# Kernel tuning notes

Measured on AMD Instinct MI355X. Metric: run time of the kernel, lower is better.

## Reference

```python
import jax, jax.numpy as jnp
import numpy as np

B, S, H, T = 64, 512, 768, 9


def setup_inputs() -> dict:
    key = jax.random.key(0)
    ks = jax.random.split(key, 8)
    embeddings = jax.random.normal(ks[0], (B, S, H), dtype=jnp.float32)
    # variable-length mask (first token always valid), as token_type_ids would give
    lengths = jax.random.randint(ks[1], (B,), 1, S + 1)
    mask = (jnp.arange(S)[None, :] < lengths[:, None]).astype(jnp.int32)
    labels = jax.random.randint(ks[2], (B, S), 0, T)
    W = jax.random.normal(ks[3], (T, H), dtype=jnp.float32) * (1.0 / np.sqrt(H))
    b = jnp.zeros((T,), dtype=jnp.float32)
    start_trans = jax.random.normal(ks[4], (T,), dtype=jnp.float32) * 0.1
    transitions = jax.random.normal(ks[5], (T, T), dtype=jnp.float32) * 0.1
    end_trans = jax.random.normal(ks[6], (T,), dtype=jnp.float32) * 0.1
    return {"embeddings": embeddings, "W": W, "b": b,
            "start_trans": start_trans, "transitions": transitions,
            "end_trans": end_trans, "labels": labels, "mask": mask}


def _crf_nll(emissions, labels, mask_bool, start_trans, transitions, end_trans):
    # emissions: [B,S,T]; returns negative log-likelihood per sequence [B]
    Bn = emissions.shape[0]
    mask_f = mask_bool.astype(emissions.dtype)
    # --- gold path score (numerator) ---
    first = start_trans[labels[:, 0]] + emissions[jnp.arange(Bn), 0, labels[:, 0]]
    emis_sc = jnp.take_along_axis(emissions, labels[..., None], axis=2)[..., 0]  # [B,S]
    trans_sc = transitions[labels[:, :-1], labels[:, 1:]]                         # [B,S-1]
    num = first + jnp.sum((emis_sc[:, 1:] + trans_sc) * mask_f[:, 1:], axis=1)
    last_idx = jnp.sum(mask_bool.astype(jnp.int32), axis=1) - 1
    last_lab = jnp.take_along_axis(labels, last_idx[:, None], axis=1)[:, 0]
    num = num + end_trans[last_lab]
    # --- log partition (forward algorithm, logsumexp recurrence) ---
    alpha0 = start_trans[None, :] + emissions[:, 0]          # [B,T]
    em_t = jnp.swapaxes(emissions, 0, 1)[1:]                 # [S-1,B,T]
    m_t = mask_bool.T[1:]                                    # [S-1,B]
    def step(alpha, xs):
        em, m = xs
        new = jax.nn.logsumexp(alpha[:, :, None] + transitions[None], axis=1) + em
        return jnp.where(m[:, None], new, alpha), None
    alpha, _ = jax.lax.scan(step, alpha0, (em_t, m_t))
    denom = jax.nn.logsumexp(alpha + end_trans[None, :], axis=1)
    return denom - num


def reference(embeddings, W, b, start_trans, transitions, end_trans, labels, mask):
    # dropout is identity at eval; Linear + ReLU emissions
    emissions = jax.nn.relu(jnp.einsum('bsh,th->bst', embeddings, W) + b)
    # -100 padding handling: zero out mask there, clamp labels to 0
    valid = labels != -100
    mask_bool = (mask != 0) & valid
    labels_mod = jnp.where(valid, labels, 0)
    nll = _crf_nll(emissions, labels_mod, mask_bool, start_trans, transitions, end_trans)
    return jnp.mean(nll)  # == -loss.mean() of the log-likelihood
```

## Files before the change

### kernel.cpp

```cpp
#include <hip/hip_runtime.h>

#define NEG_INF (-1e30f)

static constexpr int Bn = 64;
static constexpr int Sn = 512;
static constexpr int Hn = 768;
static constexpr int Tn = 9;
static constexpr int KC = 32;
static constexpr int CL = 16;
static constexpr int PSTRIDE = 108;

__device__ __forceinline__ float dot4(float4 a, float4 b) {
    return a.x * b.x + a.y * b.y + a.z * b.z + a.w * b.w;
}

__global__ __launch_bounds__(128) void fused_chunk_kernel(
        const float* __restrict__ emb, const float* __restrict__ Wm,
        const float* __restrict__ bias, const float* __restrict__ trans,
        const int* __restrict__ labels, const int* __restrict__ mask,
        float* __restrict__ chunkP, float* __restrict__ auxN,
        int* __restrict__ auxC) {
    const int bk = blockIdx.x;
    const int b  = bk >> 5;
    const int k  = bk & 31;
    const int t0 = 1 + k * CL;
    const int tid  = threadIdx.x;
    const int w    = tid >> 6;
    const int lane = tid & 63;

    __shared__ float em_s[CL][Tn];
    __shared__ int   on_s[CL];
    __shared__ float tr_s[81];

    float4 wr[Tn][3];
#pragma unroll
    for (int t = 0; t < Tn; ++t) {
        const float4* w4 = (const float4*)(Wm + t * Hn);
#pragma unroll
        for (int i = 0; i < 3; ++i) wr[t][i] = w4[lane + (i << 6)];
    }
    float bb[Tn];
#pragma unroll
    for (int t = 0; t < Tn; ++t) bb[t] = bias[t];

    if (tid < 81) tr_s[tid] = trans[tid];

    int myLab = 0, myLabP = 0, myOn = 0;
    if (tid < CL) {
        int t = t0 + tid;
        if (t < Sn) {
            int lb = labels[b * Sn + t];
            int lp = labels[b * Sn + t - 1];
            int mm = mask[b * Sn + t];
            myOn  = (mm != 0) && (lb != -100);
            myLab = (lb == -100) ? 0 : lb;
            myLabP = (lp == -100) ? 0 : lp;
        }
        on_s[tid] = myOn;
    }

#pragma unroll
    for (int rr = 0; rr < 8; ++rr) {
        const int r = w * 8 + rr;
        const int t = t0 + r;
        const int trow = (t < Sn) ? t : (Sn - 1);
        const float4* e4 = (const float4*)(emb + ((size_t)b * Sn + trow) * Hn);
        float4 e0 = e4[lane];
        float4 e1 = e4[lane + 64];
        float4 e2 = e4[lane + 128];
        float acc[Tn];
#pragma unroll
        for (int t9 = 0; t9 < Tn; ++t9)
            acc[t9] = dot4(e0, wr[t9][0]) + dot4(e1, wr[t9][1]) + dot4(e2, wr[t9][2]);
#pragma unroll
        for (int t9 = 0; t9 < Tn; ++t9) {
#pragma unroll
            for (int off = 32; off; off >>= 1)
                acc[t9] += __shfl_xor(acc[t9], off);
        }
        if (lane == 0) {
#pragma unroll
            for (int t9 = 0; t9 < Tn; ++t9)
                em_s[r][t9] = fmaxf(acc[t9] + bb[t9], 0.0f);
        }
    }
    __syncthreads();

    float nump = 0.0f;
    int cnt = 0;
    if (tid < CL && myOn) {
        nump = em_s[tid][myLab] + tr_s[myLabP * Tn + myLab];
        cnt = 1;
    }
    if (w == 0) {
#pragma unroll
        for (int off = 8; off; off >>= 1) {
            nump += __shfl_xor(nump, off);
            cnt  += __shfl_xor(cnt, off);
        }
        if (lane == 0) { auxN[bk] = nump; auxC[bk] = cnt; }
    }

    const int v  = lane / 9;
    const int jj = lane - v * 9;
    const bool act = lane < ((w == 0) ? 45 : 36);
    const int rid = (w == 0) ? v : (5 + v);

    float c[Tn];
#pragma unroll
    for (int kk = 0; kk < Tn; ++kk) c[kk] = tr_s[kk * Tn + jj];

    float pv = (act && rid == jj) ? 0.0f : NEG_INF;

    for (int u = 0; u < CL; ++u) {
        if (!on_s[u]) continue;
        float x[Tn];
#pragma unroll
        for (int kk = 0; kk < Tn; ++kk) {
            float a = __shfl(pv, (v * Tn + kk) & 63);
            x[kk] = a + c[kk];
        }
        float mx = x[0];
#pragma unroll
        for (int kk = 1; kk < Tn; ++kk) mx = fmaxf(mx, x[kk]);
        float s = 0.0f;
#pragma unroll
        for (int kk = 0; kk < Tn; ++kk) s += __expf(x[kk] - mx);
        float nv = mx + __logf(s) + em_s[u][jj];
        pv = act ? nv : pv;
    }
    if (act) chunkP[(size_t)bk * PSTRIDE + jj * 12 + rid] = pv;
}

__global__ __launch_bounds__(64) void combine_kernel(
        const float* __restrict__ emb, const float* __restrict__ Wm,
        const float* __restrict__ bias, const float* __restrict__ startT,
        const float* __restrict__ endT, const int* __restrict__ labels,
        const int* __restrict__ mask, const float* __restrict__ chunkP,
        const float* __restrict__ auxN, const int* __restrict__ auxC,
        float* __restrict__ nll) {
    const int b = blockIdx.x;
    const int lane = threadIdx.x;

    float4 wr[Tn][3];
#pragma unroll
    for (int t = 0; t < Tn; ++t) {
        const float4* w4 = (const float4*)(Wm + t * Hn);
#pragma unroll
        for (int i = 0; i < 3; ++i) wr[t][i] = w4[lane + (i << 6)];
    }
    const float4* e4 = (const float4*)(emb + (size_t)b * Sn * Hn);
    float4 e0 = e4[lane];
    float4 e1 = e4[lane + 64];
    float4 e2 = e4[lane + 128];
    float acc[Tn];
#pragma unroll
    for (int t = 0; t < Tn; ++t)
        acc[t] = dot4(e0, wr[t][0]) + dot4(e1, wr[t][1]) + dot4(e2, wr[t][2]);
#pragma unroll
    for (int t = 0; t < Tn; ++t) {
#pragma unroll
        for (int off = 32; off; off >>= 1)
            acc[t] += __shfl_xor(acc[t], off);
    }
    float em0 = NEG_INF;
#pragma unroll
    for (int t = 0; t < Tn; ++t) {
        float vt = fmaxf(acc[t] + bias[t], 0.0f);
        if (lane == t) em0 = vt;
    }
    float alpha = (lane < Tn) ? (startT[lane] + em0) : NEG_INF;

    int lab0r = labels[b * Sn];
    int lab0 = (lab0r == -100) ? 0 : lab0r;
    float first = startT[lab0] + __shfl(em0, lab0);

    float numP = (lane < KC) ? auxN[b * KC + lane] : 0.0f;
    int   cntP = (lane < KC) ? auxC[b * KC + lane] : 0;
#pragma unroll
    for (int off = 32; off; off >>= 1) {
        numP += __shfl_xor(numP, off);
        cntP += __shfl_xor(cntP, off);
    }
    int m0 = ((mask[b * Sn] != 0) && (lab0r != -100)) ? 1 : 0;
    int cntTot = cntP + m0;
    int lastIdx = cntTot - 1;
    if (lastIdx < 0) lastIdx = 0;
    int lastLab = labels[b * Sn + lastIdx];
    lastLab = (lastLab == -100) ? 0 : lastLab;
    float num = first + numP + endT[lastLab];

    const float* Pb = chunkP + (size_t)b * KC * PSTRIDE;
    float4 p0 = make_float4(0, 0, 0, 0), p1 = p0, p2 = p0;
    if (lane < Tn) {
        const float4* pp = (const float4*)(Pb + lane * 12);
        p0 = pp[0]; p1 = pp[1]; p2 = pp[2];
    }
    for (int k = 0; k < KC; ++k) {
        float4 q0 = p0, q1 = p1, q2 = p2;
        if (k + 1 < KC && lane < Tn) {
            const float4* pp = (const float4*)(Pb + (size_t)(k + 1) * PSTRIDE + lane * 12);
            p0 = pp[0]; p1 = pp[1]; p2 = pp[2];
        }
        float av[Tn];
#pragma unroll
        for (int i = 0; i < Tn; ++i) av[i] = __shfl(alpha, i);
        float x[Tn];
        x[0] = av[0] + q0.x; x[1] = av[1] + q0.y; x[2] = av[2] + q0.z;
        x[3] = av[3] + q0.w; x[4] = av[4] + q1.x; x[5] = av[5] + q1.y;
        x[6] = av[6] + q1.z; x[7] = av[7] + q1.w; x[8] = av[8] + q2.x;
        float mx = x[0];
#pragma unroll
        for (int i = 1; i < Tn; ++i) mx = fmaxf(mx, x[i]);
        float s = 0.0f;
#pragma unroll
        for (int i = 0; i < Tn; ++i) s += __expf(x[i] - mx);
        float na = mx + __logf(s);
        alpha = (lane < Tn) ? na : NEG_INF;
    }

    float z = (lane < Tn) ? (alpha + endT[lane]) : NEG_INF;
    float mx = z;
#pragma unroll
    for (int off = 32; off; off >>= 1) mx = fmaxf(mx, __shfl_xor(mx, off));
    float s = __expf(z - mx);
#pragma unroll
    for (int off = 32; off; off >>= 1) s += __shfl_xor(s, off);
    float denom = mx + __logf(s);

    if (lane == 0) nll[b] = denom - num;
}

__global__ __launch_bounds__(64) void mean_kernel(const float* __restrict__ nll,
        float* __restrict__ out) {
    float v = nll[threadIdx.x];
#pragma unroll
    for (int off = 32; off; off >>= 1) v += __shfl_xor(v, off);
    if (threadIdx.x == 0) out[0] = v * (1.0f / 64.0f);
}

extern "C" void kernel_launch(void* const* d_in, const int* in_sizes, int n_in,
                              void* d_out, int out_size, void* d_ws, size_t ws_size,
                              hipStream_t stream) {
    const float* emb    = (const float*)d_in[0];
    const float* Wm     = (const float*)d_in[1];
    const float* bias   = (const float*)d_in[2];
    const float* startT = (const float*)d_in[3];
    const float* trans  = (const float*)d_in[4];
    const float* endT   = (const float*)d_in[5];
    const int*   labels = (const int*)d_in[6];
    const int*   mask   = (const int*)d_in[7];

    float* chunkP = (float*)d_ws;
    float* auxN   = chunkP + (size_t)Bn * KC * PSTRIDE;
    int*   auxC   = (int*)(auxN + (size_t)Bn * KC);
    float* nll    = (float*)(auxC + (size_t)Bn * KC);
    float* out    = (float*)d_out;

    fused_chunk_kernel<<<Bn * KC, 128, 0, stream>>>(emb, Wm, bias, trans,
                                                    labels, mask, chunkP, auxN, auxC);
    combine_kernel<<<Bn, 64, 0, stream>>>(emb, Wm, bias, startT, endT,
                                          labels, mask, chunkP, auxN, auxC, nll);
    mean_kernel<<<1, 64, 0, stream>>>(nll, out);
}
```

Baseline: 61.05 us.

## Split emission GEMV into persistent prefetching kernel separate from CRF chunk scan

Moves the Linear+ReLU emission computation out of the chunked CRF kernel into a dedicated persistent kernel. Each wave loads W into registers once, handles two tokens per iteration, and software-prefetches the next pair's embeddings. The emissions go to a workspace buffer that the chunk and combine kernels read back. This trades an extra launch and a small emission round-trip through memory for better streaming of the 100MB embedding read and less repeated W loading.

```diff
diff --git a/kernel.cpp b/kernel.cpp
--- a/kernel.cpp
+++ b/kernel.cpp
@@ -14,12 +14,75 @@
     return a.x * b.x + a.y * b.y + a.z * b.z + a.w * b.w;
 }
 
-__global__ __launch_bounds__(128) void fused_chunk_kernel(
-        const float* __restrict__ emb, const float* __restrict__ Wm,
-        const float* __restrict__ bias, const float* __restrict__ trans,
-        const int* __restrict__ labels, const int* __restrict__ mask,
-        float* __restrict__ chunkP, float* __restrict__ auxN,
-        int* __restrict__ auxC) {
+__global__ __launch_bounds__(256) void emis_kernel(const float* __restrict__ emb,
+        const float* __restrict__ Wm, const float* __restrict__ bias,
+        float* __restrict__ em) {
+    const int lane = threadIdx.x & 63;
+    const int gw = (blockIdx.x * 256 + threadIdx.x) >> 6;
+    const int nw = (gridDim.x * 256) >> 6;
+    const int NP = (Bn * Sn) >> 1;
+
+    float4 w[Tn][3];
+#pragma unroll
+    for (int t = 0; t < Tn; ++t) {
+        const float4* w4 = (const float4*)(Wm + t * Hn);
+#pragma unroll
+        for (int i = 0; i < 3; ++i) w[t][i] = w4[lane + (i << 6)];
+    }
+    float bb[Tn];
+#pragma unroll
+    for (int t = 0; t < Tn; ++t) bb[t] = bias[t];
+
+    const int sub = (lane < 9) ? lane : (lane - 9);
+
+    float4 cA0, cA1, cA2, cB0, cB1, cB2;
+    int p = gw;
+    if (p < NP) {
+        const float4* a4 = (const float4*)(emb + (size_t)(2 * p) * Hn);
+        cA0 = a4[lane]; cA1 = a4[lane + 64]; cA2 = a4[lane + 128];
+        cB0 = a4[lane + 192]; cB1 = a4[lane + 256]; cB2 = a4[lane + 320];
+    }
+    while (p < NP) {
+        const int pn = p + nw;
+        float4 nA0, nA1, nA2, nB0, nB1, nB2;
+        if (pn < NP) {
+            const float4* a4 = (const float4*)(emb + (size_t)(2 * pn) * Hn);
+            nA0 = a4[lane]; nA1 = a4[lane + 64]; nA2 = a4[lane + 128];
+            nB0 = a4[lane + 192]; nB1 = a4[lane + 256]; nB2 = a4[lane + 320];
+        }
+        float accA[Tn], accB[Tn];
+#pragma unroll
+        for (int t = 0; t < Tn; ++t) {
+            accA[t] = dot4(cA0, w[t][0]) + dot4(cA1, w[t][1]) + dot4(cA2, w[t][2]);
+            accB[t] = dot4(cB0, w[t][0]) + dot4(cB1, w[t][1]) + dot4(cB2, w[t][2]);
+        }
+#pragma unroll
+        for (int off = 32; off; off >>= 1) {
+#pragma unroll
+            for (int t = 0; t < Tn; ++t) {
+                accA[t] += __shfl_xor(accA[t], off);
+                accB[t] += __shfl_xor(accB[t], off);
+            }
+        }
+        float outv = 0.0f;
+#pragma unroll
+        for (int t = 0; t < Tn; ++t) {
+            float va = fmaxf(accA[t] + bb[t], 0.0f);
+            float vb = fmaxf(accB[t] + bb[t], 0.0f);
+            float sel = (lane < 9) ? va : vb;
+            outv = (sub == t) ? sel : outv;
+        }
+        if (lane < 18) em[(size_t)(2 * p) * Tn + lane] = outv;
+        p = pn;
+        cA0 = nA0; cA1 = nA1; cA2 = nA2;
+        cB0 = nB0; cB1 = nB1; cB2 = nB2;
+    }
+}
+
+__global__ __launch_bounds__(128) void chunk_kernel(const float* __restrict__ em,
+        const float* __restrict__ trans, const int* __restrict__ labels,
+        const int* __restrict__ mask, float* __restrict__ chunkP,
+        float* __restrict__ auxN, int* __restrict__ auxC) {
     const int bk = blockIdx.x;
     const int b  = bk >> 5;
     const int k  = bk & 31;
@@ -31,17 +94,6 @@
     __shared__ float em_s[CL][Tn];
     __shared__ int   on_s[CL];
     __shared__ float tr_s[81];
-
-    float4 wr[Tn][3];
-#pragma unroll
-    for (int t = 0; t < Tn; ++t) {
-        const float4* w4 = (const float4*)(Wm + t * Hn);
-#pragma unroll
-        for (int i = 0; i < 3; ++i) wr[t][i] = w4[lane + (i << 6)];
-    }
-    float bb[Tn];
-#pragma unroll
-    for (int t = 0; t < Tn; ++t) bb[t] = bias[t];
 
     if (tid < 81) tr_s[tid] = trans[tid];
 
@@ -58,31 +110,10 @@
         }
         on_s[tid] = myOn;
     }
-
-#pragma unroll
-    for (int rr = 0; rr < 8; ++rr) {
-        const int r = w * 8 + rr;
-        const int t = t0 + r;
-        const int trow = (t < Sn) ? t : (Sn - 1);
-        const float4* e4 = (const float4*)(emb + ((size_t)b * Sn + trow) * Hn);
-        float4 e0 = e4[lane];
-        float4 e1 = e4[lane + 64];
-        float4 e2 = e4[lane + 128];
-        float acc[Tn];
-#pragma unroll
-        for (int t9 = 0; t9 < Tn; ++t9)
-            acc[t9] = dot4(e0, wr[t9][0]) + dot4(e1, wr[t9][1]) + dot4(e2, wr[t9][2]);
-#pragma unroll
-        for (int t9 = 0; t9 < Tn; ++t9) {
-#pragma unroll
-            for (int off = 32; off; off >>= 1)
-                acc[t9] += __shfl_xor(acc[t9], off);
-        }
-        if (lane == 0) {
-#pragma unroll
-            for (int t9 = 0; t9 < Tn; ++t9)
-                em_s[r][t9] = fmaxf(acc[t9] + bb[t9], 0.0f);
-        }
+    {
+        const int nst = (Sn - t0 < CL) ? (Sn - t0) : CL;
+        const float* src = em + (size_t)(b * Sn + t0) * Tn;
+        for (int u = tid; u < nst * Tn; u += 128) ((float*)em_s)[u] = src[u];
     }
     __syncthreads();
 
@@ -132,43 +163,15 @@
     if (act) chunkP[(size_t)bk * PSTRIDE + jj * 12 + rid] = pv;
 }
 
-__global__ __launch_bounds__(64) void combine_kernel(
-        const float* __restrict__ emb, const float* __restrict__ Wm,
-        const float* __restrict__ bias, const float* __restrict__ startT,
-        const float* __restrict__ endT, const int* __restrict__ labels,
-        const int* __restrict__ mask, const float* __restrict__ chunkP,
-        const float* __restrict__ auxN, const int* __restrict__ auxC,
-        float* __restrict__ nll) {
+__global__ __launch_bounds__(64) void combine_kernel(const float* __restrict__ em,
+        const float* __restrict__ startT, const float* __restrict__ endT,
+        const int* __restrict__ labels, const int* __restrict__ mask,
+        const float* __restrict__ chunkP, const float* __restrict__ auxN,
+        const int* __restrict__ auxC, float* __restrict__ nll) {
     const int b = blockIdx.x;
     const int lane = threadIdx.x;
 
-    float4 wr[Tn][3];
-#pragma unroll
-    for (int t = 0; t < Tn; ++t) {
-        const float4* w4 = (const float4*)(Wm + t * Hn);
-#pragma unroll
-        for (int i = 0; i < 3; ++i) wr[t][i] = w4[lane + (i << 6)];
-    }
-    const float4* e4 = (const float4*)(emb + (size_t)b * Sn * Hn);
-    float4 e0 = e4[lane];
-    float4 e1 = e4[lane + 64];
-    float4 e2 = e4[lane + 128];
-    float acc[Tn];
-#pragma unroll
-    for (int t = 0; t < Tn; ++t)
-        acc[t] = dot4(e0, wr[t][0]) + dot4(e1, wr[t][1]) + dot4(e2, wr[t][2]);
-#pragma unroll
-    for (int t = 0; t < Tn; ++t) {
-#pragma unroll
-        for (int off = 32; off; off >>= 1)
-            acc[t] += __shfl_xor(acc[t], off);
-    }
-    float em0 = NEG_INF;
-#pragma unroll
-    for (int t = 0; t < Tn; ++t) {
-        float vt = fmaxf(acc[t] + bias[t], 0.0f);
-        if (lane == t) em0 = vt;
-    }
+    float em0 = (lane < Tn) ? em[(size_t)b * Sn * Tn + lane] : NEG_INF;
     float alpha = (lane < Tn) ? (startT[lane] + em0) : NEG_INF;
 
     int lab0r = labels[b * Sn];
@@ -251,15 +254,17 @@
     const int*   labels = (const int*)d_in[6];
     const int*   mask   = (const int*)d_in[7];
 
-    float* chunkP = (float*)d_ws;
+    float* em     = (float*)d_ws;
+    float* chunkP = em + (size_t)Bn * Sn * Tn;
     float* auxN   = chunkP + (size_t)Bn * KC * PSTRIDE;
     int*   auxC   = (int*)(auxN + (size_t)Bn * KC);
     float* nll    = (float*)(auxC + (size_t)Bn * KC);
     float* out    = (float*)d_out;
 
-    fused_chunk_kernel<<<Bn * KC, 128, 0, stream>>>(emb, Wm, bias, trans,
-                                                    labels, mask, chunkP, auxN, auxC);
-    combine_kernel<<<Bn, 64, 0, stream>>>(emb, Wm, bias, startT, endT,
-                                          labels, mask, chunkP, auxN, auxC, nll);
+    emis_kernel<<<768, 256, 0, stream>>>(emb, Wm, bias, em);
+    chunk_kernel<<<Bn * KC, 128, 0, stream>>>(em, trans, labels, mask,
+                                              chunkP, auxN, auxC);
+    combine_kernel<<<Bn, 64, 0, stream>>>(em, startT, endT, labels, mask,
+                                          chunkP, auxN, auxC, nll);
     mean_kernel<<<1, 64, 0, stream>>>(nll, out);
 }
```

Result: slower. 68.99 us (+13.0%).
